# Optimization experiments

Hardware: AMD Instinct MI355X
Metric: run time of the kernel (lower is better)

## Reference

```python
import jax, jax.numpy as jnp
import numpy as np
import math

NUM_HEADS = 12
LN_EPS = 1e-5


def _band_mask(seq_len, level):
    # level 0 -> +/-2 window, level 1 -> +/-5 window, else full attention
    if level == 0:
        w = 2
    elif level == 1:
        w = 5
    else:
        return jnp.zeros((seq_len, seq_len), dtype=jnp.float32)
    i = jnp.arange(seq_len)
    inside = jnp.abs(i[:, None] - i[None, :]) <= w
    return jnp.where(inside, 0.0, -jnp.inf).astype(jnp.float32)


def setup_inputs() -> dict:
    key = jax.random.key(0)
    ks = jax.random.split(key, 8)
    B, S, H = 8, 1000, 768
    init = 0.02
    return {
        "features": jax.random.normal(ks[0], (B, S, H), jnp.float32),
        "pos_emb": jax.random.normal(ks[1], (1000, H), jnp.float32) * init,
        "Wq": jax.random.normal(ks[2], (H, H), jnp.float32) * init,
        "bq": jnp.zeros((H,), jnp.float32),
        "Wk": jax.random.normal(ks[3], (H, H), jnp.float32) * init,
        "bk": jnp.zeros((H,), jnp.float32),
        "Wv": jax.random.normal(ks[4], (H, H), jnp.float32) * init,
        "bv": jnp.zeros((H,), jnp.float32),
        "Wo": jax.random.normal(ks[5], (H, H), jnp.float32) * init,
        "bo": jnp.zeros((H,), jnp.float32),
        "ln_g": jnp.ones((H,), jnp.float32),
        "ln_b": jnp.zeros((H,), jnp.float32),
        "level": 0,
    }


def reference(features, pos_emb, Wq, bq, Wk, bk, Wv, bv, Wo, bo, ln_g, ln_b, level):
    B, S, H = features.shape
    nh = NUM_HEADS
    hd = H // nh
    # level-specific positional encoding (level_specific=True path)
    scale = 1.0 + 0.1 * level
    x = features + pos_emb[:S][None, :, :] * scale

    def proj(W, b):
        y = jnp.einsum('bsh,oh->bso', x, W) + b  # torch Linear: x @ W.T + b
        return y.reshape(B, S, nh, hd).transpose(0, 2, 1, 3)  # [B, nh, S, hd]

    Q = proj(Wq, bq)
    K = proj(Wk, bk)
    V = proj(Wv, bv)

    scores = jnp.einsum('bhqd,bhkd->bhqk', Q, K) / math.sqrt(hd)
    scores = scores + _band_mask(S, level)[None, None, :, :]
    attn = jax.nn.softmax(scores, axis=-1)  # dropout is identity (eval / p=0)
    ctx = jnp.einsum('bhqk,bhkd->bhqd', attn, V)
    ctx = ctx.transpose(0, 2, 1, 3).reshape(B, S, H)

    out = jnp.einsum('bsh,oh->bso', ctx, Wo) + bo
    y = out + features
    mu = jnp.mean(y, axis=-1, keepdims=True)
    var = jnp.var(y, axis=-1, keepdims=True)
    return (y - mu) / jnp.sqrt(var + LN_EPS) * ln_g + ln_b
```

## Files before the change

### kernel.cpp

```cpp
#include <hip/hip_runtime.h>
#include <hip/hip_bf16.h>
#include <cstddef>

typedef __attribute__((ext_vector_type(8))) short bf16x8;
typedef __attribute__((ext_vector_type(4))) float f32x4;

static __device__ __forceinline__ unsigned short f2bf(float f) {
    unsigned int u = __float_as_uint(f);
    u += 0x7fffu + ((u >> 16) & 1u);
    return (unsigned short)(u >> 16);
}
static __device__ __forceinline__ float bf2f(unsigned short h) {
    return __uint_as_float(((unsigned int)h) << 16);
}

#define B_ 8
#define S_ 1000
#define H_ 768
#define NH_ 12
#define HD_ 64
#define M_ 8000
#define HC_ 2304

__global__ __launch_bounds__(256)
void prep_all_kernel(const float* __restrict__ feat, const float* __restrict__ pos,
                     const int* __restrict__ level, unsigned short* __restrict__ xb,
                     const float* __restrict__ wq, const float* __restrict__ wk,
                     const float* __restrict__ wv, const float* __restrict__ wo,
                     unsigned short* __restrict__ wdst) {
    const size_t NX = (size_t)M_ * H_ / 4;
    const size_t WSZ = (size_t)H_ * H_;
    size_t gid = (size_t)blockIdx.x * blockDim.x + threadIdx.x;
    if (gid < NX) {
        size_t e = gid * 4;
        float sc = 1.0f + 0.1f * (float)level[0];
        const float4 f = *reinterpret_cast<const float4*>(&feat[e]);
        size_t pe = e % ((size_t)S_ * H_);
        const float4 p = *reinterpret_cast<const float4*>(&pos[pe]);
        ushort4 o;
        o.x = f2bf(f.x + sc * p.x);
        o.y = f2bf(f.y + sc * p.y);
        o.z = f2bf(f.z + sc * p.z);
        o.w = f2bf(f.w + sc * p.w);
        *reinterpret_cast<ushort4*>(&xb[e]) = o;
    } else {
        size_t e = (gid - NX) * 4;
        if (e >= 4 * WSZ) return;
        const float* src; size_t off;
        if (e < WSZ)          { src = wq; off = e; }
        else if (e < 2 * WSZ) { src = wk; off = e - WSZ; }
        else if (e < 3 * WSZ) { src = wv; off = e - 2 * WSZ; }
        else                  { src = wo; off = e - 3 * WSZ; }
        const float4 f = *reinterpret_cast<const float4*>(&src[off]);
        ushort4 o;
        o.x = f2bf(f.x); o.y = f2bf(f.y); o.z = f2bf(f.z); o.w = f2bf(f.w);
        *reinterpret_cast<ushort4*>(&wdst[e]) = o;
    }
}

#define BM 128
#define BN 128
#define BK 32

template<int EPI>
__global__ __launch_bounds__(256)
void gemm_bt_kernel(const unsigned short* __restrict__ A,
                    const unsigned short* __restrict__ B,
                    int M, int N, int K,
                    const float* __restrict__ b0, const float* __restrict__ b1,
                    const float* __restrict__ b2,
                    const float* __restrict__ resid,
                    unsigned short* __restrict__ outB, float* __restrict__ outF) {
    __shared__ bf16x8 lds8[2048];
    char* ldsb = (char*)lds8;
    const int tid  = threadIdx.x;
    const int lane = tid & 63;
    const int wid  = tid >> 6;
    const int wm = wid >> 1, wn = wid & 1;
    const int fr = lane & 15, fq = lane >> 4;

    const int nwg = gridDim.x;
    const int q = nwg >> 3, r = nwg & 7;
    const int xcd = blockIdx.x & 7, idx = blockIdx.x >> 3;
    const int swz = (xcd < r) ? (xcd * (q + 1) + idx) : (r * (q + 1) + (xcd - r) * q + idx);
    const int ntn = N / BN;
    const int bm = (swz / ntn) * BM;
    const int bn = (swz % ntn) * BN;

    const int srow = lane >> 2;
    const int scol = ((lane & 3) ^ ((lane >> 3) & 3)) * 8;

    auto stage = [&](int buf, int k0) {
        char* base = ldsb + buf * 16384;
#pragma unroll
        for (int t = 0; t < 2; ++t) {
            const int c = wid * 2 + t;
            const int rr = c * 16 + srow;
            int ar = bm + rr;
            ar = ar < M ? ar : M - 1;
            const unsigned short* ga = A + (size_t)ar * K + k0 + scol;
            __builtin_amdgcn_global_load_lds(
                (const __attribute__((address_space(1))) unsigned int*)ga,
                (__attribute__((address_space(3))) unsigned int*)(base + c * 1024), 16, 0, 0);
            const int br = bn + rr;
            const unsigned short* gb = B + (size_t)br * K + k0 + scol;
            __builtin_amdgcn_global_load_lds(
                (const __attribute__((address_space(1))) unsigned int*)gb,
                (__attribute__((address_space(3))) unsigned int*)(base + 8192 + c * 1024), 16, 0, 0);
        }
    };

    f32x4 acc[4][4] = {};
    const int NT = K / BK;

    stage(0, 0);
    for (int t = 0; t < NT; ++t) {
        const int cur = t & 1;
        if (t + 1 < NT) {
            stage(cur ^ 1, (t + 1) * BK);
            asm volatile("s_waitcnt vmcnt(4)" ::: "memory");
        } else {
            asm volatile("s_waitcnt vmcnt(0)" ::: "memory");
        }
        __builtin_amdgcn_s_barrier();

        char* base = ldsb + cur * 16384;
        bf16x8 af[4], bfv[4];
#pragma unroll
        for (int m = 0; m < 4; ++m) {
            const int row = wm * 64 + m * 16 + fr;
            const int slot = fq ^ ((fr >> 1) & 3);
            af[m] = *reinterpret_cast<const bf16x8*>(base + row * 64 + slot * 16);
        }
#pragma unroll
        for (int n = 0; n < 4; ++n) {
            const int row = wn * 64 + n * 16 + fr;
            const int slot = fq ^ ((fr >> 1) & 3);
            bfv[n] = *reinterpret_cast<const bf16x8*>(base + 8192 + row * 64 + slot * 16);
        }
#pragma unroll
        for (int m = 0; m < 4; ++m)
#pragma unroll
            for (int n = 0; n < 4; ++n)
                acc[m][n] = __builtin_amdgcn_mfma_f32_16x16x32_bf16(af[m], bfv[n], acc[m][n], 0, 0, 0);
        __builtin_amdgcn_s_barrier();
    }

#pragma unroll
    for (int m = 0; m < 4; ++m) {
#pragma unroll
        for (int n = 0; n < 4; ++n) {
            int col = bn + wn * 64 + n * 16 + fr;
#pragma unroll
            for (int j = 0; j < 4; ++j) {
                int row = bm + wm * 64 + m * 16 + fq * 4 + j;
                if (row >= M) continue;
                float v = acc[m][n][j];
                if (EPI == 0) {
                    float bias = (col < 768) ? b0[col] : (col < 1536) ? b1[col - 768] : b2[col - 1536];
                    outB[(size_t)row * N + col] = f2bf(v + bias);
                } else {
                    v += b0[col] + resid[(size_t)row * N + col];
                    outF[(size_t)row * N + col] = v;
                }
            }
        }
    }
}

__global__ __launch_bounds__(256)
void attn_kernel(const unsigned short* __restrict__ QKV,
                 unsigned short* __restrict__ ctx,
                 const int* __restrict__ level_p) {
    const int lane = threadIdx.x & 63;
    const int wv = threadIdx.x >> 6;
    const int qiw = lane >> 2;
    const int d0 = (lane & 3) * 16;

    const int qt = blockIdx.x & 15;
    const int h  = (blockIdx.x >> 4) % NH_;
    const int b  = blockIdx.x / (16 * NH_);
    const int i  = qt * 64 + wv * 16 + qiw;
    const bool valid = i < S_;
    const int iq = valid ? i : S_ - 1;

    const int lev = level_p[0];
    const int w = (lev == 0) ? 2 : (lev == 1) ? 5 : S_;

    const size_t qoff = (size_t)(b * S_ + iq) * HC_ + h * HD_ + d0;
    bf16x8 qa = *reinterpret_cast<const bf16x8*>(&QKV[qoff]);
    bf16x8 qb = *reinterpret_cast<const bf16x8*>(&QKV[qoff + 8]);
    float qf[16];
#pragma unroll
    for (int t = 0; t < 8; ++t) {
        qf[t]     = bf2f((unsigned short)qa[t]);
        qf[t + 8] = bf2f((unsigned short)qb[t]);
    }

    const int j0 = max(0, i - w), j1 = min(S_ - 1, i + w);
    float mx = -1e30f, l = 0.f;
    float acc[16];
#pragma unroll
    for (int t = 0; t < 16; ++t) acc[t] = 0.f;

    for (int jc = j0; jc <= j1; jc += 5) {
        float s[5];
        int jj[5];
#pragma unroll
        for (int t = 0; t < 5; ++t) {
            const int j = jc + t;
            jj[t] = j <= j1 ? j : j1;
            const size_t koff = (size_t)(b * S_ + jj[t]) * HC_ + 768 + h * HD_ + d0;
            bf16x8 ka = *reinterpret_cast<const bf16x8*>(&QKV[koff]);
            bf16x8 kb = *reinterpret_cast<const bf16x8*>(&QKV[koff + 8]);
            float p = 0.f;
#pragma unroll
            for (int d = 0; d < 8; ++d) {
                p = fmaf(qf[d], bf2f((unsigned short)ka[d]), p);
                p = fmaf(qf[d + 8], bf2f((unsigned short)kb[d]), p);
            }
            s[t] = p;
        }
#pragma unroll
        for (int t = 0; t < 5; ++t) s[t] += __shfl_xor(s[t], 1);
#pragma unroll
        for (int t = 0; t < 5; ++t) s[t] += __shfl_xor(s[t], 2);
#pragma unroll
        for (int t = 0; t < 5; ++t)
            s[t] = (jc + t <= j1) ? s[t] * 0.125f : -1e30f;

        float cm = fmaxf(fmaxf(fmaxf(s[0], s[1]), fmaxf(s[2], s[3])), s[4]);
        float nm = fmaxf(mx, cm);
        float corr = __expf(mx - nm);
        l *= corr;
#pragma unroll
        for (int t = 0; t < 16; ++t) acc[t] *= corr;
#pragma unroll
        for (int t = 0; t < 5; ++t) {
            const float e = __expf(s[t] - nm);
            l += e;
            const size_t voff = (size_t)(b * S_ + jj[t]) * HC_ + 1536 + h * HD_ + d0;
            bf16x8 va = *reinterpret_cast<const bf16x8*>(&QKV[voff]);
            bf16x8 vb = *reinterpret_cast<const bf16x8*>(&QKV[voff + 8]);
#pragma unroll
            for (int d = 0; d < 8; ++d) {
                acc[d]     = fmaf(e, bf2f((unsigned short)va[d]), acc[d]);
                acc[d + 8] = fmaf(e, bf2f((unsigned short)vb[d]), acc[d + 8]);
            }
        }
        mx = nm;
    }

    if (valid) {
        const float inv = 1.f / l;
        bf16x8 o0, o1;
#pragma unroll
        for (int t = 0; t < 8; ++t) {
            o0[t] = (short)f2bf(acc[t] * inv);
            o1[t] = (short)f2bf(acc[t + 8] * inv);
        }
        unsigned short* dst = &ctx[(size_t)(b * S_ + i) * H_ + h * HD_ + d0];
        *reinterpret_cast<bf16x8*>(dst) = o0;
        *reinterpret_cast<bf16x8*>(dst + 8) = o1;
    }
}

__global__ __launch_bounds__(256)
void ln_kernel(float* __restrict__ y, const float* __restrict__ g, const float* __restrict__ bta) {
    int row = blockIdx.x;
    int tid = threadIdx.x;
    float* p = y + (size_t)row * H_;
    float v[3];
    float s = 0.f, s2 = 0.f;
#pragma unroll
    for (int t = 0; t < 3; ++t) {
        v[t] = p[tid + t * 256];
        s += v[t];
        s2 += v[t] * v[t];
    }
#pragma unroll
    for (int o = 32; o; o >>= 1) {
        s  += __shfl_xor(s, o);
        s2 += __shfl_xor(s2, o);
    }
    __shared__ float ss[4], ss2[4];
    if ((tid & 63) == 0) { ss[tid >> 6] = s; ss2[tid >> 6] = s2; }
    __syncthreads();
    s  = ss[0] + ss[1] + ss[2] + ss[3];
    s2 = ss2[0] + ss2[1] + ss2[2] + ss2[3];
    float mu = s * (1.f / H_);
    float var = s2 * (1.f / H_) - mu * mu;
    float rs = rsqrtf(var + 1e-5f);
#pragma unroll
    for (int t = 0; t < 3; ++t) {
        int c = tid + t * 256;
        p[c] = (v[t] - mu) * rs * g[c] + bta[c];
    }
}

extern "C" void kernel_launch(void* const* d_in, const int* in_sizes, int n_in,
                              void* d_out, int out_size, void* d_ws, size_t ws_size,
                              hipStream_t stream) {
    const float* feat  = (const float*)d_in[0];
    const float* pos   = (const float*)d_in[1];
    const float* Wq    = (const float*)d_in[2];
    const float* bq    = (const float*)d_in[3];
    const float* Wk    = (const float*)d_in[4];
    const float* bk    = (const float*)d_in[5];
    const float* Wv    = (const float*)d_in[6];
    const float* bv    = (const float*)d_in[7];
    const float* Wo    = (const float*)d_in[8];
    const float* bo    = (const float*)d_in[9];
    const float* ln_g  = (const float*)d_in[10];
    const float* ln_b  = (const float*)d_in[11];
    const int*   level = (const int*)d_in[12];
    float* out = (float*)d_out;

    char* ws = (char*)d_ws;
    unsigned short* xb   = (unsigned short*)ws;
    unsigned short* Wcat = xb + (size_t)M_ * H_;
    unsigned short* QKVb = Wcat + (size_t)4 * H_ * H_;
    unsigned short* ctxb = QKVb + (size_t)M_ * HC_;

    const int nprep = (int)(((size_t)M_ * H_ / 4 + (size_t)4 * H_ * H_ / 4 + 255) / 256);
    prep_all_kernel<<<nprep, 256, 0, stream>>>(feat, pos, level, xb, Wq, Wk, Wv, Wo, Wcat);
    gemm_bt_kernel<0><<<(HC_ / BN) * ((M_ + BM - 1) / BM), 256, 0, stream>>>(
        xb, Wcat, M_, HC_, H_, bq, bk, bv, nullptr, QKVb, nullptr);
    attn_kernel<<<B_ * NH_ * 16, 256, 0, stream>>>(QKVb, ctxb, level);
    gemm_bt_kernel<1><<<(H_ / BN) * ((M_ + BM - 1) / BM), 256, 0, stream>>>(
        ctxb, Wcat + (size_t)3 * H_ * H_, M_, H_, H_, bo, nullptr, nullptr, feat, nullptr, out);
    ln_kernel<<<M_, 256, 0, stream>>>(out, ln_g, ln_b);
}
```

Measured before the change: 127.1 us.

## Add 256x256-tile 8-phase pipelined QKV GEMM with async LDS loads

Replaces the generic 128x128 QKV projection GEMM with a dedicated 512-thread kernel using 256x256 output tiles, a 128KB LDS multi-buffer fed by global_load_lds, and an interleaved schedule of LDS reads, MFMA bursts with raised priority, and barriers. It aims to raise data reuse per tile and overlap global loads with matrix math. The remaining output GEMM is specialised into its own kernel without the epilogue template. Risks include lower occupancy from the large LDS footprint, a fixed grid of 288 blocks that is not a multiple of the CU count (tail imbalance), and hand-tuned waitcnt correctness.

```diff
diff --git a/kernel.cpp b/kernel.cpp
--- a/kernel.cpp
+++ b/kernel.cpp
@@ -58,19 +58,141 @@
     }
 }
 
+#define QK_ 768
+
+__global__ __launch_bounds__(512, 2)
+void gemm_qkv_8ph(const unsigned short* __restrict__ A,
+                  const unsigned short* __restrict__ Bw,
+                  const float* __restrict__ b0, const float* __restrict__ b1,
+                  const float* __restrict__ b2,
+                  unsigned short* __restrict__ outB) {
+    __shared__ char lds[131072];
+    const int tid = threadIdx.x, lane = tid & 63, wid = tid >> 6;
+    const int wr = wid >> 2, wc = wid & 3;
+    const int fr = lane & 15, fq = lane >> 4;
+
+    const int swz = (blockIdx.x & 7) * 36 + (blockIdx.x >> 3);
+    const int bm = (swz / 9) * 256, bn = (swz % 9) * 256;
+
+    const int srow = lane >> 2;
+    const int scol = ((lane & 3) ^ ((lane >> 3) & 3)) * 8;
+
+    auto ST = [&](int slot, const unsigned short* Mx, int rb, int kc, int rmax) {
+        char* base = lds + slot * 16384;
+#pragma unroll
+        for (int t = 0; t < 2; ++t) {
+            const int c = wid * 2 + t;
+            int r = rb + c * 16 + srow;
+            r = r < rmax ? r : rmax - 1;
+            __builtin_amdgcn_global_load_lds(
+                (const __attribute__((address_space(1))) unsigned int*)(Mx + (size_t)r * QK_ + kc + scol),
+                (__attribute__((address_space(3))) unsigned int*)(base + c * 1024), 16, 0, 0);
+        }
+    };
+
+    f32x4 acc[8][4] = {};
+    bf16x8 af[4], bfv[4];
+    const int rsl = fq ^ ((fr >> 1) & 3);
+
+    auto RA = [&](int kt, int mh, int ks) {
+        char* base = lds + ((kt & 1) * 4 + ks) * 16384;
+#pragma unroll
+        for (int q = 0; q < 4; ++q) {
+            const int row = wr * 128 + (mh * 4 + q) * 16 + fr;
+            af[q] = *reinterpret_cast<const bf16x8*>(base + row * 64 + rsl * 16);
+        }
+    };
+    auto RB = [&](int kt, int ks) {
+        char* base = lds + ((kt & 1) * 4 + 2 + ks) * 16384;
+#pragma unroll
+        for (int n = 0; n < 4; ++n) {
+            const int row = wc * 64 + n * 16 + fr;
+            bfv[n] = *reinterpret_cast<const bf16x8*>(base + row * 64 + rsl * 16);
+        }
+    };
+    auto MF = [&](int mh) {
+        __builtin_amdgcn_s_setprio(1);
+#pragma unroll
+        for (int q = 0; q < 4; ++q)
+#pragma unroll
+            for (int n = 0; n < 4; ++n)
+                acc[mh * 4 + q][n] = __builtin_amdgcn_mfma_f32_16x16x32_bf16(
+                    af[q], bfv[n], acc[mh * 4 + q][n], 0, 0, 0);
+        __builtin_amdgcn_s_setprio(0);
+    };
+
+    ST(0, A, bm, 0, M_);  ST(2, Bw, bn, 0, HC_);
+    ST(1, A, bm, 32, M_); ST(3, Bw, bn, 32, HC_);
+    ST(4, A, bm, 64, M_); ST(6, Bw, bn, 64, HC_);
+    asm volatile("s_waitcnt vmcnt(4)" ::: "memory");
+    __builtin_amdgcn_s_barrier();
+
+    for (int i = 0; i < 6; ++i) {
+        const int a = 2 * i, b = 2 * i + 1;
+        const bool last = (i == 5);
+        const int ka = a * 64, kb = b * 64;
+        RA(a, 0, 0); RB(a, 0);
+        ST(5, A, bm, kb + 32, M_); ST(7, Bw, bn, kb + 32, HC_);
+        asm volatile("" ::: "memory"); __builtin_amdgcn_s_barrier();
+        MF(0);
+        RA(a, 1, 0);
+        asm volatile("" ::: "memory"); __builtin_amdgcn_s_barrier();
+        MF(1);
+        RA(a, 0, 1); RB(a, 1);
+        if (!last) ST(0, A, bm, ka + 128, M_);
+        asm volatile("" ::: "memory"); __builtin_amdgcn_s_barrier();
+        MF(0);
+        RA(a, 1, 1);
+        if (!last) ST(2, Bw, bn, ka + 128, HC_);
+        if (last) { asm volatile("s_waitcnt vmcnt(0)" ::: "memory"); }
+        else      { asm volatile("s_waitcnt vmcnt(4)" ::: "memory"); }
+        __builtin_amdgcn_s_barrier();
+        MF(1);
+        RA(b, 0, 0); RB(b, 0);
+        if (!last) { ST(1, A, bm, ka + 160, M_); ST(3, Bw, bn, ka + 160, HC_); }
+        asm volatile("" ::: "memory"); __builtin_amdgcn_s_barrier();
+        MF(0);
+        RA(b, 1, 0);
+        asm volatile("" ::: "memory"); __builtin_amdgcn_s_barrier();
+        MF(1);
+        RA(b, 0, 1); RB(b, 1);
+        if (!last) ST(4, A, bm, kb + 128, M_);
+        asm volatile("" ::: "memory"); __builtin_amdgcn_s_barrier();
+        MF(0);
+        RA(b, 1, 1);
+        if (!last) ST(6, Bw, bn, kb + 128, HC_);
+        if (last) { asm volatile("s_waitcnt vmcnt(0)" ::: "memory"); }
+        else      { asm volatile("s_waitcnt vmcnt(4)" ::: "memory"); }
+        __builtin_amdgcn_s_barrier();
+        MF(1);
+    }
+
+#pragma unroll
+    for (int m = 0; m < 8; ++m) {
+#pragma unroll
+        for (int n = 0; n < 4; ++n) {
+            const int col = bn + wc * 64 + n * 16 + fr;
+            const float bias = (col < 768) ? b0[col] : (col < 1536) ? b1[col - 768] : b2[col - 1536];
+#pragma unroll
+            for (int j = 0; j < 4; ++j) {
+                const int row = bm + wr * 128 + m * 16 + fq * 4 + j;
+                if (row < M_) outB[(size_t)row * HC_ + col] = f2bf(acc[m][n][j] + bias);
+            }
+        }
+    }
+}
+
 #define BM 128
 #define BN 128
 #define BK 32
 
-template<int EPI>
 __global__ __launch_bounds__(256)
-void gemm_bt_kernel(const unsigned short* __restrict__ A,
-                    const unsigned short* __restrict__ B,
-                    int M, int N, int K,
-                    const float* __restrict__ b0, const float* __restrict__ b1,
-                    const float* __restrict__ b2,
-                    const float* __restrict__ resid,
-                    unsigned short* __restrict__ outB, float* __restrict__ outF) {
+void gemm_out_kernel(const unsigned short* __restrict__ A,
+                     const unsigned short* __restrict__ B,
+                     const float* __restrict__ b0,
+                     const float* __restrict__ resid,
+                     float* __restrict__ outF) {
+    const int M = M_, N = H_, K = H_;
     __shared__ bf16x8 lds8[2048];
     char* ldsb = (char*)lds8;
     const int tid  = threadIdx.x;
@@ -155,14 +277,8 @@
             for (int j = 0; j < 4; ++j) {
                 int row = bm + wm * 64 + m * 16 + fq * 4 + j;
                 if (row >= M) continue;
-                float v = acc[m][n][j];
-                if (EPI == 0) {
-                    float bias = (col < 768) ? b0[col] : (col < 1536) ? b1[col - 768] : b2[col - 1536];
-                    outB[(size_t)row * N + col] = f2bf(v + bias);
-                } else {
-                    v += b0[col] + resid[(size_t)row * N + col];
-                    outF[(size_t)row * N + col] = v;
-                }
+                float v = acc[m][n][j] + b0[col] + resid[(size_t)row * N + col];
+                outF[(size_t)row * N + col] = v;
             }
         }
     }
@@ -324,10 +440,9 @@
 
     const int nprep = (int)(((size_t)M_ * H_ / 4 + (size_t)4 * H_ * H_ / 4 + 255) / 256);
     prep_all_kernel<<<nprep, 256, 0, stream>>>(feat, pos, level, xb, Wq, Wk, Wv, Wo, Wcat);
-    gemm_bt_kernel<0><<<(HC_ / BN) * ((M_ + BM - 1) / BM), 256, 0, stream>>>(
-        xb, Wcat, M_, HC_, H_, bq, bk, bv, nullptr, QKVb, nullptr);
+    gemm_qkv_8ph<<<288, 512, 0, stream>>>(xb, Wcat, bq, bk, bv, QKVb);
     attn_kernel<<<B_ * NH_ * 16, 256, 0, stream>>>(QKVb, ctxb, level);
-    gemm_bt_kernel<1><<<(H_ / BN) * ((M_ + BM - 1) / BM), 256, 0, stream>>>(
-        ctxb, Wcat + (size_t)3 * H_ * H_, M_, H_, H_, bo, nullptr, nullptr, feat, nullptr, out);
+    gemm_out_kernel<<<(H_ / BN) * ((M_ + BM - 1) / BM), 256, 0, stream>>>(
+        ctxb, Wcat + (size_t)3 * H_ * H_, bo, feat, out);
     ln_kernel<<<M_, 256, 0, stream>>>(out, ln_g, ln_b);
 }
```

Measured after the change: 145.2 us. 1.14x slower.

## Specialize QKV and output GEMMs with new wave tiling and vectorized epilogues

Applied to the files above, without the earlier changes.

Replaces the templated GEMM with two specialized kernels. The QKV kernel runs 8 waves per 128x128 tile, each wave computing a 64x32 subtile. The output GEMM uses 128x64 tiles, which gives more blocks for the N=768 case. Both swap the MFMA operands so each lane holds four consecutive columns, which lets the epilogue do vectorized bias, residual and bf16 stores. Both also add s_setprio around the MFMA block, trading register reuse per wave for more waves and better occupancy.

```diff
diff --git a/kernel.cpp b/kernel.cpp
--- a/kernel.cpp
+++ b/kernel.cpp
@@ -58,112 +58,193 @@
     }
 }
 
-#define BM 128
-#define BN 128
-#define BK 32
-
-template<int EPI>
-__global__ __launch_bounds__(256)
-void gemm_bt_kernel(const unsigned short* __restrict__ A,
-                    const unsigned short* __restrict__ B,
-                    int M, int N, int K,
-                    const float* __restrict__ b0, const float* __restrict__ b1,
-                    const float* __restrict__ b2,
-                    const float* __restrict__ resid,
-                    unsigned short* __restrict__ outB, float* __restrict__ outF) {
-    __shared__ bf16x8 lds8[2048];
-    char* ldsb = (char*)lds8;
-    const int tid  = threadIdx.x;
-    const int lane = tid & 63;
-    const int wid  = tid >> 6;
-    const int wm = wid >> 1, wn = wid & 1;
+__global__ __launch_bounds__(512, 4)
+void gemm_qkv2(const unsigned short* __restrict__ A,
+               const unsigned short* __restrict__ Bw,
+               const float* __restrict__ b0, const float* __restrict__ b1,
+               const float* __restrict__ b2,
+               unsigned short* __restrict__ outB) {
+    const int K = H_;
+    __shared__ char lds[32768];
+    const int tid = threadIdx.x, lane = tid & 63, wid = tid >> 6;
+    const int wr = wid >> 2, wc = wid & 3;
     const int fr = lane & 15, fq = lane >> 4;
 
     const int nwg = gridDim.x;
     const int q = nwg >> 3, r = nwg & 7;
     const int xcd = blockIdx.x & 7, idx = blockIdx.x >> 3;
     const int swz = (xcd < r) ? (xcd * (q + 1) + idx) : (r * (q + 1) + (xcd - r) * q + idx);
-    const int ntn = N / BN;
-    const int bm = (swz / ntn) * BM;
-    const int bn = (swz % ntn) * BN;
+    const int ntn = HC_ / 128;
+    const int bm = (swz / ntn) * 128;
+    const int bn = (swz % ntn) * 128;
 
     const int srow = lane >> 2;
     const int scol = ((lane & 3) ^ ((lane >> 3) & 3)) * 8;
 
     auto stage = [&](int buf, int k0) {
-        char* base = ldsb + buf * 16384;
-#pragma unroll
-        for (int t = 0; t < 2; ++t) {
-            const int c = wid * 2 + t;
-            const int rr = c * 16 + srow;
-            int ar = bm + rr;
-            ar = ar < M ? ar : M - 1;
-            const unsigned short* ga = A + (size_t)ar * K + k0 + scol;
-            __builtin_amdgcn_global_load_lds(
-                (const __attribute__((address_space(1))) unsigned int*)ga,
-                (__attribute__((address_space(3))) unsigned int*)(base + c * 1024), 16, 0, 0);
-            const int br = bn + rr;
-            const unsigned short* gb = B + (size_t)br * K + k0 + scol;
-            __builtin_amdgcn_global_load_lds(
-                (const __attribute__((address_space(1))) unsigned int*)gb,
-                (__attribute__((address_space(3))) unsigned int*)(base + 8192 + c * 1024), 16, 0, 0);
-        }
+        char* base = lds + buf * 16384;
+        const int c = wid;
+        int ar = bm + c * 16 + srow;
+        ar = ar < M_ ? ar : M_ - 1;
+        __builtin_amdgcn_global_load_lds(
+            (const __attribute__((address_space(1))) unsigned int*)(A + (size_t)ar * K + k0 + scol),
+            (__attribute__((address_space(3))) unsigned int*)(base + c * 1024), 16, 0, 0);
+        const int br = bn + c * 16 + srow;
+        __builtin_amdgcn_global_load_lds(
+            (const __attribute__((address_space(1))) unsigned int*)(Bw + (size_t)br * K + k0 + scol),
+            (__attribute__((address_space(3))) unsigned int*)(base + 8192 + c * 1024), 16, 0, 0);
     };
 
-    f32x4 acc[4][4] = {};
-    const int NT = K / BK;
+    f32x4 acc[4][2] = {};
+    const int rsl = fq ^ ((fr >> 1) & 3);
+    const int NT = K / 32;
 
     stage(0, 0);
     for (int t = 0; t < NT; ++t) {
         const int cur = t & 1;
         if (t + 1 < NT) {
-            stage(cur ^ 1, (t + 1) * BK);
-            asm volatile("s_waitcnt vmcnt(4)" ::: "memory");
+            stage(cur ^ 1, (t + 1) * 32);
+            asm volatile("s_waitcnt vmcnt(2)" ::: "memory");
         } else {
             asm volatile("s_waitcnt vmcnt(0)" ::: "memory");
         }
         __builtin_amdgcn_s_barrier();
 
-        char* base = ldsb + cur * 16384;
-        bf16x8 af[4], bfv[4];
+        char* base = lds + cur * 16384;
+        bf16x8 af[4], bfv[2];
 #pragma unroll
         for (int m = 0; m < 4; ++m) {
-            const int row = wm * 64 + m * 16 + fr;
-            const int slot = fq ^ ((fr >> 1) & 3);
-            af[m] = *reinterpret_cast<const bf16x8*>(base + row * 64 + slot * 16);
-        }
-#pragma unroll
-        for (int n = 0; n < 4; ++n) {
-            const int row = wn * 64 + n * 16 + fr;
-            const int slot = fq ^ ((fr >> 1) & 3);
-            bfv[n] = *reinterpret_cast<const bf16x8*>(base + 8192 + row * 64 + slot * 16);
-        }
+            const int row = wr * 64 + m * 16 + fr;
+            af[m] = *reinterpret_cast<const bf16x8*>(base + row * 64 + rsl * 16);
+        }
+#pragma unroll
+        for (int n = 0; n < 2; ++n) {
+            const int row = wc * 32 + n * 16 + fr;
+            bfv[n] = *reinterpret_cast<const bf16x8*>(base + 8192 + row * 64 + rsl * 16);
+        }
+        __builtin_amdgcn_s_setprio(1);
 #pragma unroll
         for (int m = 0; m < 4; ++m)
 #pragma unroll
-            for (int n = 0; n < 4; ++n)
-                acc[m][n] = __builtin_amdgcn_mfma_f32_16x16x32_bf16(af[m], bfv[n], acc[m][n], 0, 0, 0);
+            for (int n = 0; n < 2; ++n)
+                acc[m][n] = __builtin_amdgcn_mfma_f32_16x16x32_bf16(bfv[n], af[m], acc[m][n], 0, 0, 0);
+        __builtin_amdgcn_s_setprio(0);
         __builtin_amdgcn_s_barrier();
     }
 
+    const int colg = (bn < 768) ? bn : (bn < 1536) ? bn - 768 : bn - 1536;
+    const float* bsel = (bn < 768) ? b0 : (bn < 1536) ? b1 : b2;
 #pragma unroll
     for (int m = 0; m < 4; ++m) {
-#pragma unroll
-        for (int n = 0; n < 4; ++n) {
-            int col = bn + wn * 64 + n * 16 + fr;
-#pragma unroll
-            for (int j = 0; j < 4; ++j) {
-                int row = bm + wm * 64 + m * 16 + fq * 4 + j;
-                if (row >= M) continue;
-                float v = acc[m][n][j];
-                if (EPI == 0) {
-                    float bias = (col < 768) ? b0[col] : (col < 1536) ? b1[col - 768] : b2[col - 1536];
-                    outB[(size_t)row * N + col] = f2bf(v + bias);
-                } else {
-                    v += b0[col] + resid[(size_t)row * N + col];
-                    outF[(size_t)row * N + col] = v;
-                }
-            }
+        const int row = bm + wr * 64 + m * 16 + fr;
+        if (row >= M_) continue;
+#pragma unroll
+        for (int n = 0; n < 2; ++n) {
+            const int cb = wc * 32 + n * 16 + fq * 4;
+            const float4 bv = *reinterpret_cast<const float4*>(&bsel[colg + cb]);
+            ushort4 o;
+            o.x = f2bf(acc[m][n][0] + bv.x);
+            o.y = f2bf(acc[m][n][1] + bv.y);
+            o.z = f2bf(acc[m][n][2] + bv.z);
+            o.w = f2bf(acc[m][n][3] + bv.w);
+            *reinterpret_cast<ushort4*>(&outB[(size_t)row * HC_ + bn + cb]) = o;
+        }
+    }
+}
+
+__global__ __launch_bounds__(256, 4)
+void gemm_out2(const unsigned short* __restrict__ A,
+               const unsigned short* __restrict__ Bw,
+               const float* __restrict__ b0,
+               const float* __restrict__ resid,
+               float* __restrict__ outF) {
+    const int K = H_;
+    __shared__ char lds[24576];
+    const int tid = threadIdx.x, lane = tid & 63, wid = tid >> 6;
+    const int wr = wid >> 1, wc = wid & 1;
+    const int fr = lane & 15, fq = lane >> 4;
+
+    const int nwg = gridDim.x;
+    const int q = nwg >> 3, r = nwg & 7;
+    const int xcd = blockIdx.x & 7, idx = blockIdx.x >> 3;
+    const int swz = (xcd < r) ? (xcd * (q + 1) + idx) : (r * (q + 1) + (xcd - r) * q + idx);
+    const int ntn = H_ / 64;
+    const int bm = (swz / ntn) * 128;
+    const int bn = (swz % ntn) * 64;
+
+    const int srow = lane >> 2;
+    const int scol = ((lane & 3) ^ ((lane >> 3) & 3)) * 8;
+
+    auto stage = [&](int buf, int k0) {
+        char* base = lds + buf * 12288;
+#pragma unroll
+        for (int t = 0; t < 2; ++t) {
+            const int c = wid * 2 + t;
+            int ar = bm + c * 16 + srow;
+            ar = ar < M_ ? ar : M_ - 1;
+            __builtin_amdgcn_global_load_lds(
+                (const __attribute__((address_space(1))) unsigned int*)(A + (size_t)ar * K + k0 + scol),
+                (__attribute__((address_space(3))) unsigned int*)(base + c * 1024), 16, 0, 0);
+        }
+        const int c = wid;
+        const int br = bn + c * 16 + srow;
+        __builtin_amdgcn_global_load_lds(
+            (const __attribute__((address_space(1))) unsigned int*)(Bw + (size_t)br * K + k0 + scol),
+            (__attribute__((address_space(3))) unsigned int*)(base + 8192 + c * 1024), 16, 0, 0);
+    };
+
+    f32x4 acc[4][2] = {};
+    const int rsl = fq ^ ((fr >> 1) & 3);
+    const int NT = K / 32;
+
+    stage(0, 0);
+    for (int t = 0; t < NT; ++t) {
+        const int cur = t & 1;
+        if (t + 1 < NT) {
+            stage(cur ^ 1, (t + 1) * 32);
+            asm volatile("s_waitcnt vmcnt(3)" ::: "memory");
+        } else {
+            asm volatile("s_waitcnt vmcnt(0)" ::: "memory");
+        }
+        __builtin_amdgcn_s_barrier();
+
+        char* base = lds + cur * 12288;
+        bf16x8 af[4], bfv[2];
+#pragma unroll
+        for (int m = 0; m < 4; ++m) {
+            const int row = wr * 64 + m * 16 + fr;
+            af[m] = *reinterpret_cast<const bf16x8*>(base + row * 64 + rsl * 16);
+        }
+#pragma unroll
+        for (int n = 0; n < 2; ++n) {
+            const int row = wc * 32 + n * 16 + fr;
+            bfv[n] = *reinterpret_cast<const bf16x8*>(base + 8192 + row * 64 + rsl * 16);
+        }
+        __builtin_amdgcn_s_setprio(1);
+#pragma unroll
+        for (int m = 0; m < 4; ++m)
+#pragma unroll
+            for (int n = 0; n < 2; ++n)
+                acc[m][n] = __builtin_amdgcn_mfma_f32_16x16x32_bf16(bfv[n], af[m], acc[m][n], 0, 0, 0);
+        __builtin_amdgcn_s_setprio(0);
+        __builtin_amdgcn_s_barrier();
+    }
+
+#pragma unroll
+    for (int m = 0; m < 4; ++m) {
+        const int row = bm + wr * 64 + m * 16 + fr;
+        if (row >= M_) continue;
+#pragma unroll
+        for (int n = 0; n < 2; ++n) {
+            const int col = bn + wc * 32 + n * 16 + fq * 4;
+            const float4 bv = *reinterpret_cast<const float4*>(&b0[col]);
+            const float4 rv = *reinterpret_cast<const float4*>(&resid[(size_t)row * H_ + col]);
+            float4 ov;
+            ov.x = acc[m][n][0] + bv.x + rv.x;
+            ov.y = acc[m][n][1] + bv.y + rv.y;
+            ov.z = acc[m][n][2] + bv.z + rv.z;
+            ov.w = acc[m][n][3] + bv.w + rv.w;
+            *reinterpret_cast<float4*>(&outF[(size_t)row * H_ + col]) = ov;
         }
     }
 }
@@ -324,10 +405,8 @@
 
     const int nprep = (int)(((size_t)M_ * H_ / 4 + (size_t)4 * H_ * H_ / 4 + 255) / 256);
     prep_all_kernel<<<nprep, 256, 0, stream>>>(feat, pos, level, xb, Wq, Wk, Wv, Wo, Wcat);
-    gemm_bt_kernel<0><<<(HC_ / BN) * ((M_ + BM - 1) / BM), 256, 0, stream>>>(
-        xb, Wcat, M_, HC_, H_, bq, bk, bv, nullptr, QKVb, nullptr);
+    gemm_qkv2<<<63 * 18, 512, 0, stream>>>(xb, Wcat, bq, bk, bv, QKVb);
     attn_kernel<<<B_ * NH_ * 16, 256, 0, stream>>>(QKVb, ctxb, level);
-    gemm_bt_kernel<1><<<(H_ / BN) * ((M_ + BM - 1) / BM), 256, 0, stream>>>(
-        ctxb, Wcat + (size_t)3 * H_ * H_, M_, H_, H_, bo, nullptr, nullptr, feat, nullptr, out);
+    gemm_out2<<<63 * 12, 256, 0, stream>>>(ctxb, Wcat + (size_t)3 * H_ * H_, bo, feat, out);
     ln_kernel<<<M_, 256, 0, stream>>>(out, ln_g, ln_b);
 }
```

Measured after the change: 110.0 us. 13.5% less time.
